# Kernel tuning notes

Measured on AMD Instinct MI355X. Metric: run time of the kernel, lower is better.

Reference implementation:

```python
import jax, jax.numpy as jnp
import numpy as np

HEADS = 16
HIDDEN = 1024
HEAD_DIM = HIDDEN // HEADS


def setup_inputs() -> dict:
    key = jax.random.key(0)
    ks = jax.random.split(key, 12)
    B, S, H = 2, 2048, HIDDEN
    scale = 1.0 / np.sqrt(H)
    inp = {
        'q': jax.random.normal(ks[0], (B, S, H), jnp.float32),
        'k': jax.random.normal(ks[1], (B, S, H), jnp.float32),
        'v': jax.random.normal(ks[2], (B, S, H), jnp.float32),
        'mask': jnp.ones((B, S), jnp.int32),
        'Wq': jax.random.normal(ks[3], (H, H), jnp.float32) * scale,
        'bq': jnp.zeros((H,), jnp.float32),
        'Wk': jax.random.normal(ks[4], (H, H), jnp.float32) * scale,
        'bk': jnp.zeros((H,), jnp.float32),
        'Wv': jax.random.normal(ks[5], (H, H), jnp.float32) * scale,
        'bv': jnp.zeros((H,), jnp.float32),
        'Wo': jax.random.normal(ks[6], (H, H), jnp.float32) * scale,
        'bo': jnp.zeros((H,), jnp.float32),
    }
    return inp


def reference(q, k, v, mask, Wq, bq, Wk, bk, Wv, bv, Wo, bo):
    B, S, H = q.shape
    hd = HEAD_DIM
    # projections (torch Linear: x @ W.T + b) -> [B, heads, S, hd]
    qh = (q @ Wq.T + bq).reshape(B, S, HEADS, hd).transpose(0, 2, 1, 3)
    kh = (k @ Wk.T + bk).reshape(B, S, HEADS, hd).transpose(0, 2, 1, 3)
    vh = (v @ Wv.T + bv).reshape(B, S, HEADS, hd).transpose(0, 2, 1, 3)
    # full score matrix [B, heads, Sq, Sk]
    scores = jnp.einsum('bhqd,bhkd->bhqk', qh, kh) / np.sqrt(hd)
    # mask [B, Sq] -> [B, 1, Sq, 1], masks entire query rows where mask==0
    m = mask[:, None, :, None]
    scores = jnp.where(m == 0, jnp.float32(-1e9), scores)
    attn = jax.nn.softmax(scores, axis=-1)
    # dropout omitted (eval mode / deterministic)
    y = jnp.einsum('bhqk,bhkd->bhqd', attn, vh)
    y = y.transpose(0, 2, 1, 3).reshape(B, S, H)
    return y @ Wo.T + bo
```

## Files before the change

### kernel.cpp

```cpp
#include <hip/hip_runtime.h>
#include <hip/hip_bf16.h>
#include <cstdint>

#define EL 1048576ull

typedef __bf16 bf16_t;
typedef bf16_t bf16x8 __attribute__((ext_vector_type(8)));
typedef float  f32x4  __attribute__((ext_vector_type(4)));
typedef unsigned int u32x2 __attribute__((ext_vector_type(2)));
typedef unsigned int u32x4 __attribute__((ext_vector_type(4)));

__device__ __forceinline__ unsigned short f2bf(float f) {
  unsigned int u = __builtin_bit_cast(unsigned int, f);
  u += 0x7FFFu + ((u >> 16) & 1u);
  return (unsigned short)(u >> 16);
}

__device__ __forceinline__ unsigned int cvtpk(float lo, float hi2) {
  unsigned int r;
  asm("v_cvt_pk_bf16_f32 %0, %1, %2" : "=v"(r) : "v"(lo), "v"(hi2));
  return r;
}

__device__ __forceinline__ float fexp2(float x) {
#if __has_builtin(__builtin_amdgcn_exp2f)
  return __builtin_amdgcn_exp2f(x);
#else
  return exp2f(x);
#endif
}

typedef __attribute__((address_space(1))) void as1_void;
typedef __attribute__((address_space(3))) void as3_void;
__device__ __forceinline__ void load_lds16(const void* g, void* l) {
  __builtin_amdgcn_global_load_lds((as1_void*)g, (as3_void*)l, 16, 0, 0);
}

__device__ __forceinline__ bf16x8 repack_af(const f32x4 s0v, const f32x4 s1v) {
  unsigned int c00 = cvtpk(s0v[0], s0v[1]);
  unsigned int c01 = cvtpk(s0v[2], s0v[3]);
  unsigned int c10 = cvtpk(s1v[0], s1v[1]);
  unsigned int c11 = cvtpk(s1v[2], s1v[3]);
  asm("v_permlane32_swap_b32 %0, %1" : "+v"(c00), "+v"(c10));
  asm("v_permlane16_swap_b32 %0, %1" : "+v"(c00), "+v"(c10));
  asm("v_permlane32_swap_b32 %0, %1" : "+v"(c01), "+v"(c11));
  asm("v_permlane16_swap_b32 %0, %1" : "+v"(c01), "+v"(c11));
  u32x4 wd; wd[0] = c00; wd[1] = c01; wd[2] = c10; wd[3] = c11;
  return __builtin_bit_cast(bf16x8, wd);
}

__global__ __launch_bounds__(256) void convert_all(
    const float* __restrict__ q, const float* __restrict__ k, const float* __restrict__ v,
    const float* __restrict__ wq, const float* __restrict__ wk,
    const float* __restrict__ wv, const float* __restrict__ wo,
    unsigned short* __restrict__ ws)
{
  const size_t total_v4 = 4 * EL;
  for (size_t v4 = (size_t)blockIdx.x * blockDim.x + threadIdx.x; v4 < total_v4;
       v4 += (size_t)gridDim.x * blockDim.x) {
    size_t e = v4 * 4;
    unsigned seg = (unsigned)(e >> 20);
    const float* s; size_t base;
    if      (seg < 4)   { s = q;  base = 0; }
    else if (seg < 8)   { s = k;  base = 4*EL; }
    else if (seg < 12)  { s = v;  base = 8*EL; }
    else if (seg == 12) { s = wq; base = 12*EL; }
    else if (seg == 13) { s = wk; base = 13*EL; }
    else if (seg == 14) { s = wv; base = 14*EL; }
    else                { s = wo; base = 15*EL; }
    const float4 f = *(const float4*)(s + (e - base));
    ushort4 o;
    o.x = f2bf(f.x); o.y = f2bf(f.y); o.z = f2bf(f.z); o.w = f2bf(f.w);
    *(ushort4*)(ws + e) = o;
  }
}

template <int BM, int BN, int WM, int WN>
__device__ __forceinline__ void gemm_bt_main(
    const unsigned short* __restrict__ A,
    const unsigned short* __restrict__ B,
    f32x4 (&acc)[BM / WM / 16][BN / WN / 16],
    const int tm, const int tn)
{
  constexpr int K = 1024, BK = 64;
  constexpr int AM = BM / WM / 16, AN = BN / WN / 16;
  __shared__ __align__(16) unsigned short sA[BM * BK];
  __shared__ __align__(16) unsigned short sB[BN * BK];
  const int tid  = threadIdx.x;
  const int wave = tid >> 6, lane = tid & 63;
  const int wm = wave / WN, wn = wave % WN;
  const int l16 = lane & 15, hi = lane >> 4, swz = l16 & 7;

  for (int k0 = 0; k0 < K; k0 += BK) {
    __syncthreads();
#pragma unroll
    for (int i = 0; i < BM * 8 / 256; i++) {
      int p = i * 256 + tid;
      int row = p >> 3, c = p & 7;
      load_lds16(A + (size_t)(tm + row) * K + k0 + ((c ^ (row & 7)) * 8),
                 &sA[(i * 256 + wave * 64) * 8]);
    }
#pragma unroll
    for (int i = 0; i < BN * 8 / 256; i++) {
      int p = i * 256 + tid;
      int row = p >> 3, c = p & 7;
      load_lds16(B + (size_t)(tn + row) * K + k0 + ((c ^ (row & 7)) * 8),
                 &sB[(i * 256 + wave * 64) * 8]);
    }
    __syncthreads();

#pragma unroll
    for (int kk = 0; kk < 2; kk++) {
      bf16x8 af[AM], bfr[AN];
#pragma unroll
      for (int i = 0; i < AM; i++) {
        int row = wm * (BM / WM) + i * 16 + l16;
        af[i] = *(const bf16x8*)&sA[row * BK + (((kk * 4 + hi) ^ swz) * 8)];
      }
#pragma unroll
      for (int j = 0; j < AN; j++) {
        int row = wn * (BN / WN) + j * 16 + l16;
        bfr[j] = *(const bf16x8*)&sB[row * BK + (((kk * 4 + hi) ^ swz) * 8)];
      }
#pragma unroll
      for (int i = 0; i < AM; i++)
#pragma unroll
        for (int j = 0; j < AN; j++)
          acc[i][j] = __builtin_amdgcn_mfma_f32_16x16x32_bf16(af[i], bfr[j], acc[i][j], 0, 0, 0);
    }
  }
}

__global__ __launch_bounds__(256, 3) void qkv_gemm(
    const unsigned short* qb, const unsigned short* kb, const unsigned short* vb,
    const unsigned short* wqb, const unsigned short* wkb, const unsigned short* wvb,
    const float* bq, const float* bk, const float* bv,
    unsigned short* Qp, unsigned short* Kp, unsigned short* Vt)
{
  const unsigned short* A; const unsigned short* B; const float* bias;
  if (blockIdx.z == 0)      { A = qb; B = wqb; bias = bq; }
  else if (blockIdx.z == 1) { A = kb; B = wkb; bias = bk; }
  else                      { A = vb; B = wvb; bias = bv; }

  const int xd = blockIdx.x, yd = blockIdx.y;
  const int mt = xd + 8 * (yd & 3);
  const int nt = yd >> 2;
  const int tm = mt * 128, tn = nt * 128;

  f32x4 acc[4][4] = {};
  gemm_bt_main<128, 128, 2, 2>(A, B, acc, tm, tn);

  const int tid = threadIdx.x, wave = tid >> 6, lane = tid & 63;
  const int wm = wave >> 1, wn = wave & 1;
  const int l16 = lane & 15, hi = lane >> 4;

  if (blockIdx.z < 2) {
    unsigned short* C = (blockIdx.z == 0) ? Qp : Kp;
    const float scale = (blockIdx.z == 0) ? 0.18033688011112042f : 1.0f;
#pragma unroll
    for (int i = 0; i < 4; i++) {
      int row0 = tm + wm * 64 + i * 16 + hi * 4;
#pragma unroll
      for (int j = 0; j < 4; j++) {
        int col = tn + wn * 64 + j * 16 + l16;
        float bv2 = bias[col];
#pragma unroll
        for (int r = 0; r < 4; r++)
          C[(size_t)(row0 + r) * 1024 + col] = f2bf((acc[i][j][r] + bv2) * scale);
      }
    }
  } else {
#pragma unroll
    for (int i = 0; i < 4; i++) {
      int row0 = tm + wm * 64 + i * 16 + hi * 4;
      int bb = row0 >> 11, s = row0 & 2047;
#pragma unroll
      for (int j = 0; j < 4; j++) {
        int col = tn + wn * 64 + j * 16 + l16;
        int hh = col >> 6, d = col & 63;
        float bv2 = bias[col];
        u32x2 w;
        w[0] = cvtpk(acc[i][j][0] + bv2, acc[i][j][1] + bv2);
        w[1] = cvtpk(acc[i][j][2] + bv2, acc[i][j][3] + bv2);
        *(u32x2*)&Vt[((size_t)(bb * 16 + hh) * 64 + d) * 2048 + s] = w;
      }
    }
  }
}

__global__ __launch_bounds__(256, 2) void out_gemm(
    const unsigned short* Yb, const unsigned short* wob, const float* bo, float* out)
{
  const int xd = blockIdx.x, yd = blockIdx.y;
  const int mt = (xd & 7) + 8 * (yd & 3);
  const int nt = (xd >> 3) + 2 * (yd >> 2);
  const int tm = mt * 128, tn = nt * 64;

  f32x4 acc[2][4] = {};
  gemm_bt_main<128, 64, 4, 1>(Yb, wob, acc, tm, tn);

  const int tid = threadIdx.x, wave = tid >> 6, lane = tid & 63;
  const int l16 = lane & 15, hi = lane >> 4;
#pragma unroll
  for (int i = 0; i < 2; i++) {
    int row0 = tm + wave * 32 + i * 16 + hi * 4;
#pragma unroll
    for (int j = 0; j < 4; j++) {
      int col = tn + j * 16 + l16;
      float bv2 = bo[col];
#pragma unroll
      for (int r = 0; r < 4; r++)
        out[(size_t)(row0 + r) * 1024 + col] = acc[i][j][r] + bv2;
    }
  }
}

__global__ __launch_bounds__(256, 2) void attn_kernel(
    const unsigned short* __restrict__ Qp, const unsigned short* __restrict__ Kp,
    const unsigned short* __restrict__ Vt, const int* __restrict__ mask,
    unsigned short* __restrict__ Yb)
{
  constexpr int S = 2048, H = 1024;
  __shared__ __align__(16) unsigned short sK[2][128 * 64];
  __shared__ __align__(16) unsigned short sV[2][64 * 128];

  const int tid = threadIdx.x, wave = tid >> 6, lane = tid & 63;
  const int l16 = lane & 15, hi = lane >> 4, swz = l16 & 7;
  const int xd = blockIdx.x, hd = blockIdx.y;
  const int h  = (xd & 7) + 8 * (hd & 1);
  const int qt = ((xd >> 3) + 2 * (hd >> 1)) * 128;
  const int b = blockIdx.z, bh = b * 16 + h;
  const unsigned short* Qb = Qp + (size_t)b * S * H + (size_t)h * 64;
  const unsigned short* Kb = Kp + (size_t)b * S * H + (size_t)h * 64;
  const unsigned short* Vb = Vt + (size_t)bh * 64 * 2048;

  const int kinv0 = l16 * 64 + ((hi ^ swz) * 8);
  const int kinv1 = l16 * 64 + (((4 + hi) ^ swz) * 8);
  const int vinv0 = l16 * 128 + ((hi ^ swz) * 8);
  const int vinv1 = l16 * 128 + (((4 + hi) ^ swz) * 8);

#pragma unroll
  for (int i = 0; i < 4; i++) {
    int p = i * 256 + tid, row = p >> 3, c = p & 7;
    load_lds16(Qb + (size_t)(qt + row) * H + ((c ^ (row & 7)) * 8),
               &sK[1][(i * 256 + wave * 64) * 8]);
  }
  const unsigned short* pK[4]; const unsigned short* pV[4];
#pragma unroll
  for (int j = 0; j < 4; j++) {
    int g = j * 256 + tid;
    int row = g >> 3, c = g & 7;
    pK[j] = Kb + (size_t)row * H + ((c ^ (row & 7)) * 8);
    int d = g >> 4, kvc = g & 15;
    int sg = ((kvc ^ d) & 7) | (kvc & 8);
    pV[j] = Vb + (size_t)d * 2048 + sg * 8;
  }
#pragma unroll
  for (int j = 0; j < 4; j++)
    load_lds16(pK[j], &sK[0][(j * 256 + wave * 64) * 8]);
#pragma unroll
  for (int j = 0; j < 4; j++)
    load_lds16(pV[j], &sV[0][(j * 256 + wave * 64) * 8]);
#pragma unroll
  for (int j = 0; j < 4; j++) { pK[j] += 128 * H; pV[j] += 128; }

  asm volatile("s_waitcnt vmcnt(8)" ::: "memory");
  __builtin_amdgcn_sched_barrier(0);
  __builtin_amdgcn_s_barrier();

  bf16x8 qf[2][2];
#pragma unroll
  for (int m = 0; m < 2; m++) {
    const int row = wave * 32 + m * 16 + l16;
    const int qm = mask[(size_t)b * S + qt + row];
#pragma unroll
    for (int ks = 0; ks < 2; ks++) {
      bf16x8 v = *(const bf16x8*)&sK[1][row * 64 + (((ks * 4 + hi) ^ swz) * 8)];
      u32x4 u = __builtin_bit_cast(u32x4, v);
#pragma unroll
      for (int c = 0; c < 4; c++) u[c] = qm ? u[c] : 0u;
      qf[m][ks] = __builtin_bit_cast(bf16x8, u);
    }
  }
  asm volatile("s_waitcnt lgkmcnt(0)" ::: "memory");
  __builtin_amdgcn_sched_barrier(0);
  __builtin_amdgcn_s_barrier();

  float lsum[2] = {0.f, 0.f};
  f32x4 oacc[2][4] = {};

  for (int t = 0; t < 16; t++) {
    const int cur = t & 1;
    if (t < 15) {
      unsigned short* nK = sK[cur ^ 1];
      unsigned short* nV = sV[cur ^ 1];
#pragma unroll
      for (int j = 0; j < 4; j++)
        load_lds16(pK[j], &nK[(j * 256 + wave * 64) * 8]);
#pragma unroll
      for (int j = 0; j < 4; j++)
        load_lds16(pV[j], &nV[(j * 256 + wave * 64) * 8]);
#pragma unroll
      for (int j = 0; j < 4; j++) { pK[j] += 128 * H; pV[j] += 128; }
      asm volatile("s_waitcnt vmcnt(8)" ::: "memory");
    } else {
      asm volatile("s_waitcnt vmcnt(0)" ::: "memory");
    }
    __builtin_amdgcn_sched_barrier(0);
    __builtin_amdgcn_s_barrier();

    const unsigned short* kb = sK[cur];
    const unsigned short* vb = sV[cur];

#pragma unroll
    for (int hf = 0; hf < 2; hf++) {
      f32x4 sf[2][4];
      __builtin_amdgcn_s_setprio(1);
#pragma unroll
      for (int jj = 0; jj < 4; jj++) {
        const int ro = (hf * 4 + jj) * 1024;
        bf16x8 kf0 = *(const bf16x8*)&kb[ro + kinv0];
        bf16x8 kf1 = *(const bf16x8*)&kb[ro + kinv1];
#pragma unroll
        for (int m = 0; m < 2; m++) {
          f32x4 acc = {-16.0f, -16.0f, -16.0f, -16.0f};
          acc = __builtin_amdgcn_mfma_f32_16x16x32_bf16(kf0, qf[m][0], acc, 0, 0, 0);
          acc = __builtin_amdgcn_mfma_f32_16x16x32_bf16(kf1, qf[m][1], acc, 0, 0, 0);
          sf[m][jj] = acc;
        }
      }
      __builtin_amdgcn_s_setprio(0);

#pragma unroll
      for (int m = 0; m < 2; m++) {
#pragma unroll
        for (int jj = 0; jj < 4; jj++)
#pragma unroll
          for (int r = 0; r < 4; r++)
            sf[m][jj][r] = fexp2(sf[m][jj][r]);
        f32x4 c4 = (sf[m][0] + sf[m][1]) + (sf[m][2] + sf[m][3]);
        lsum[m] += (c4[0] + c4[1]) + (c4[2] + c4[3]);
      }

#pragma unroll
      for (int w2 = 0; w2 < 2; w2++) {
        bf16x8 af0 = repack_af(sf[0][2 * w2], sf[0][2 * w2 + 1]);
        bf16x8 af1 = repack_af(sf[1][2 * w2], sf[1][2 * w2 + 1]);
        const int gw = hf * 2 + w2;
        const int vo = ((gw & 2) ? 64 : 0) + ((gw & 1) ? vinv1 : vinv0);
        __builtin_amdgcn_s_setprio(1);
#pragma unroll
        for (int n = 0; n < 4; n++) {
          bf16x8 vf = *(const bf16x8*)&vb[n * 2048 + vo];
          oacc[0][n] = __builtin_amdgcn_mfma_f32_16x16x32_bf16(af0, vf, oacc[0][n], 0, 0, 0);
          oacc[1][n] = __builtin_amdgcn_mfma_f32_16x16x32_bf16(af1, vf, oacc[1][n], 0, 0, 0);
        }
        __builtin_amdgcn_s_setprio(0);
      }
    }
    __builtin_amdgcn_sched_barrier(0);
    __builtin_amdgcn_s_barrier();
  }

#pragma unroll
  for (int m = 0; m < 2; m++) {
    lsum[m] += __shfl_xor(lsum[m], 16);
    lsum[m] += __shfl_xor(lsum[m], 32);
  }
#pragma unroll
  for (int m = 0; m < 2; m++) {
    float lr[4];
#pragma unroll
    for (int r = 0; r < 4; r++) lr[r] = 1.0f / __shfl(lsum[m], hi * 4 + r);
#pragma unroll
    for (int n = 0; n < 4; n++)
#pragma unroll
      for (int r = 0; r < 4; r++) {
        int row = qt + wave * 32 + m * 16 + hi * 4 + r;
        int col = n * 16 + l16;
        Yb[((size_t)b * S + row) * H + h * 64 + col] = f2bf(oacc[m][n][r] * lr[r]);
      }
  }
}

extern "C" void kernel_launch(void* const* d_in, const int* in_sizes, int n_in,
                              void* d_out, int out_size, void* d_ws, size_t ws_size,
                              hipStream_t stream)
{
  const float* q  = (const float*)d_in[0];
  const float* k  = (const float*)d_in[1];
  const float* v  = (const float*)d_in[2];
  const int*  mask = (const int*)d_in[3];
  const float* Wq = (const float*)d_in[4];
  const float* bq = (const float*)d_in[5];
  const float* Wk = (const float*)d_in[6];
  const float* bk = (const float*)d_in[7];
  const float* Wv = (const float*)d_in[8];
  const float* bv = (const float*)d_in[9];
  const float* Wo = (const float*)d_in[10];
  const float* bo = (const float*)d_in[11];

  unsigned short* ws  = (unsigned short*)d_ws;
  unsigned short* qb  = ws;
  unsigned short* kb  = ws + 4 * EL;
  unsigned short* vb  = ws + 8 * EL;
  unsigned short* wqb = ws + 12 * EL;
  unsigned short* wkb = ws + 13 * EL;
  unsigned short* wvb = ws + 14 * EL;
  unsigned short* wob = ws + 15 * EL;
  unsigned short* Qp  = ws + 16 * EL;
  unsigned short* Kp  = ws + 20 * EL;
  unsigned short* Vt  = ws + 24 * EL;
  unsigned short* Yb  = ws + 28 * EL;

  convert_all<<<2048, 256, 0, stream>>>(q, k, v, Wq, Wk, Wv, Wo, ws);
  qkv_gemm<<<dim3(8, 32, 3), 256, 0, stream>>>(qb, kb, vb, wqb, wkb, wvb,
                                               bq, bk, bv, Qp, Kp, Vt);
  attn_kernel<<<dim3(16, 16, 2), 256, 0, stream>>>(Qp, Kp, Vt, mask, Yb);
  out_gemm<<<dim3(16, 32), 256, 0, stream>>>(Yb, wob, bo, (float*)d_out);
}
```

Measured before the change: 108.3 us.

## Split attention KV sequence across two wave groups with LDS reduction

Doubles the attention block to 512 threads: two groups of four waves each process half of the key/value sequence for the same 128-query tile, using per-half 64-row double-buffered K/V tiles in LDS. At the end, the second half writes its partial output and row sums to shared memory and the first half combines them before normalising and writing bf16 output. This aims to raise per-CU wave parallelism and latency hiding for the attention loop, at the cost of an extra LDS reduction, a block-wide sync and higher register/LDS pressure per block, which may limit occupancy.

```diff
diff --git a/kernel.cpp b/kernel.cpp
--- a/kernel.cpp
+++ b/kernel.cpp
@@ -215,17 +215,18 @@
   }
 }
 
-__global__ __launch_bounds__(256, 2) void attn_kernel(
+__global__ __launch_bounds__(512, 2) void attn_kernel(
     const unsigned short* __restrict__ Qp, const unsigned short* __restrict__ Kp,
     const unsigned short* __restrict__ Vt, const int* __restrict__ mask,
     unsigned short* __restrict__ Yb)
 {
   constexpr int S = 2048, H = 1024;
-  __shared__ __align__(16) unsigned short sK[2][128 * 64];
-  __shared__ __align__(16) unsigned short sV[2][64 * 128];
+  __shared__ __align__(16) unsigned short smem[32768];
 
   const int tid = threadIdx.x, wave = tid >> 6, lane = tid & 63;
   const int l16 = lane & 15, hi = lane >> 4, swz = l16 & 7;
+  const int half = wave >> 2, w4 = wave & 3;
+  const int kvoff = half * 1024;
   const int xd = blockIdx.x, hd = blockIdx.y;
   const int h  = (xd & 7) + 8 * (hd & 1);
   const int qt = ((xd >> 3) + 2 * (hd >> 1)) * 128;
@@ -234,48 +235,59 @@
   const unsigned short* Kb = Kp + (size_t)b * S * H + (size_t)h * 64;
   const unsigned short* Vb = Vt + (size_t)bh * 64 * 2048;
 
+  unsigned short* sK0 = smem + (half * 2) * 4096;
+  unsigned short* sK1 = smem + (half * 2 + 1) * 4096;
+  unsigned short* sV0 = smem + 16384 + (half * 2) * 4096;
+  unsigned short* sV1 = smem + 16384 + (half * 2 + 1) * 4096;
+
   const int kinv0 = l16 * 64 + ((hi ^ swz) * 8);
   const int kinv1 = l16 * 64 + (((4 + hi) ^ swz) * 8);
-  const int vinv0 = l16 * 128 + ((hi ^ swz) * 8);
-  const int vinv1 = l16 * 128 + (((4 + hi) ^ swz) * 8);
-
-#pragma unroll
-  for (int i = 0; i < 4; i++) {
-    int p = i * 256 + tid, row = p >> 3, c = p & 7;
-    load_lds16(Qb + (size_t)(qt + row) * H + ((c ^ (row & 7)) * 8),
-               &sK[1][(i * 256 + wave * 64) * 8]);
-  }
-  const unsigned short* pK[4]; const unsigned short* pV[4];
-#pragma unroll
-  for (int j = 0; j < 4; j++) {
-    int g = j * 256 + tid;
+  const int vinv0 = kinv0, vinv1 = kinv1;
+
+  {
+    unsigned short* qdst0 = smem + 4096;
+    unsigned short* qdst1 = smem + 12288;
+#pragma unroll
+    for (int i = 0; i < 2; i++) {
+      int p = i * 512 + tid, row = p >> 3, c = p & 7;
+      load_lds16(Qb + (size_t)(qt + row) * H + ((c ^ (row & 7)) * 8),
+                 &(i ? qdst1 : qdst0)[(wave * 64) * 8]);
+    }
+  }
+  const int htid = tid & 255;
+  const unsigned short* pK[2]; const unsigned short* pV[2];
+#pragma unroll
+  for (int j = 0; j < 2; j++) {
+    int g = j * 256 + htid;
     int row = g >> 3, c = g & 7;
-    pK[j] = Kb + (size_t)row * H + ((c ^ (row & 7)) * 8);
-    int d = g >> 4, kvc = g & 15;
-    int sg = ((kvc ^ d) & 7) | (kvc & 8);
-    pV[j] = Vb + (size_t)d * 2048 + sg * 8;
-  }
-#pragma unroll
-  for (int j = 0; j < 4; j++)
-    load_lds16(pK[j], &sK[0][(j * 256 + wave * 64) * 8]);
-#pragma unroll
-  for (int j = 0; j < 4; j++)
-    load_lds16(pV[j], &sV[0][(j * 256 + wave * 64) * 8]);
-#pragma unroll
-  for (int j = 0; j < 4; j++) { pK[j] += 128 * H; pV[j] += 128; }
-
-  asm volatile("s_waitcnt vmcnt(8)" ::: "memory");
+    pK[j] = Kb + (size_t)(kvoff + row) * H + ((c ^ (row & 7)) * 8);
+    int d = g >> 3, kvc = g & 7;
+    int sg = kvc ^ (d & 7);
+    pV[j] = Vb + (size_t)d * 2048 + kvoff + sg * 8;
+  }
+#pragma unroll
+  for (int j = 0; j < 2; j++)
+    load_lds16(pK[j], &sK0[(j * 256 + w4 * 64) * 8]);
+#pragma unroll
+  for (int j = 0; j < 2; j++)
+    load_lds16(pV[j], &sV0[(j * 256 + w4 * 64) * 8]);
+#pragma unroll
+  for (int j = 0; j < 2; j++) { pK[j] += 64 * H; pV[j] += 64; }
+
+  asm volatile("s_waitcnt vmcnt(4)" ::: "memory");
   __builtin_amdgcn_sched_barrier(0);
   __builtin_amdgcn_s_barrier();
 
   bf16x8 qf[2][2];
 #pragma unroll
   for (int m = 0; m < 2; m++) {
-    const int row = wave * 32 + m * 16 + l16;
+    const int row = w4 * 32 + m * 16 + l16;
     const int qm = mask[(size_t)b * S + qt + row];
+    const unsigned short* qsrc = (row < 64) ? (smem + 4096 + row * 64)
+                                            : (smem + 12288 + (row - 64) * 64);
 #pragma unroll
     for (int ks = 0; ks < 2; ks++) {
-      bf16x8 v = *(const bf16x8*)&sK[1][row * 64 + (((ks * 4 + hi) ^ swz) * 8)];
+      bf16x8 v = *(const bf16x8*)&qsrc[((ks * 4 + hi) ^ swz) * 8];
       u32x4 u = __builtin_bit_cast(u32x4, v);
 #pragma unroll
       for (int c = 0; c < 4; c++) u[c] = qm ? u[c] : 0u;
@@ -292,71 +304,67 @@
   for (int t = 0; t < 16; t++) {
     const int cur = t & 1;
     if (t < 15) {
-      unsigned short* nK = sK[cur ^ 1];
-      unsigned short* nV = sV[cur ^ 1];
-#pragma unroll
-      for (int j = 0; j < 4; j++)
-        load_lds16(pK[j], &nK[(j * 256 + wave * 64) * 8]);
-#pragma unroll
-      for (int j = 0; j < 4; j++)
-        load_lds16(pV[j], &nV[(j * 256 + wave * 64) * 8]);
-#pragma unroll
-      for (int j = 0; j < 4; j++) { pK[j] += 128 * H; pV[j] += 128; }
-      asm volatile("s_waitcnt vmcnt(8)" ::: "memory");
+      unsigned short* nK = cur ? sK0 : sK1;
+      unsigned short* nV = cur ? sV0 : sV1;
+#pragma unroll
+      for (int j = 0; j < 2; j++)
+        load_lds16(pK[j], &nK[(j * 256 + w4 * 64) * 8]);
+#pragma unroll
+      for (int j = 0; j < 2; j++)
+        load_lds16(pV[j], &nV[(j * 256 + w4 * 64) * 8]);
+#pragma unroll
+      for (int j = 0; j < 2; j++) { pK[j] += 64 * H; pV[j] += 64; }
+      asm volatile("s_waitcnt vmcnt(4)" ::: "memory");
     } else {
       asm volatile("s_waitcnt vmcnt(0)" ::: "memory");
     }
     __builtin_amdgcn_sched_barrier(0);
     __builtin_amdgcn_s_barrier();
 
-    const unsigned short* kb = sK[cur];
-    const unsigned short* vb = sV[cur];
-
-#pragma unroll
-    for (int hf = 0; hf < 2; hf++) {
-      f32x4 sf[2][4];
+    const unsigned short* kb = cur ? sK1 : sK0;
+    const unsigned short* vb = cur ? sV1 : sV0;
+
+    f32x4 sf[2][4];
+    __builtin_amdgcn_s_setprio(1);
+#pragma unroll
+    for (int jj = 0; jj < 4; jj++) {
+      const int ro = jj * 1024;
+      bf16x8 kf0 = *(const bf16x8*)&kb[ro + kinv0];
+      bf16x8 kf1 = *(const bf16x8*)&kb[ro + kinv1];
+#pragma unroll
+      for (int m = 0; m < 2; m++) {
+        f32x4 acc = {-16.0f, -16.0f, -16.0f, -16.0f};
+        acc = __builtin_amdgcn_mfma_f32_16x16x32_bf16(kf0, qf[m][0], acc, 0, 0, 0);
+        acc = __builtin_amdgcn_mfma_f32_16x16x32_bf16(kf1, qf[m][1], acc, 0, 0, 0);
+        sf[m][jj] = acc;
+      }
+    }
+    __builtin_amdgcn_s_setprio(0);
+
+#pragma unroll
+    for (int m = 0; m < 2; m++) {
+#pragma unroll
+      for (int jj = 0; jj < 4; jj++)
+#pragma unroll
+        for (int r = 0; r < 4; r++)
+          sf[m][jj][r] = fexp2(sf[m][jj][r]);
+      f32x4 c4 = (sf[m][0] + sf[m][1]) + (sf[m][2] + sf[m][3]);
+      lsum[m] += (c4[0] + c4[1]) + (c4[2] + c4[3]);
+    }
+
+#pragma unroll
+    for (int w2 = 0; w2 < 2; w2++) {
+      bf16x8 af0 = repack_af(sf[0][2 * w2], sf[0][2 * w2 + 1]);
+      bf16x8 af1 = repack_af(sf[1][2 * w2], sf[1][2 * w2 + 1]);
+      const int vo = w2 ? vinv1 : vinv0;
       __builtin_amdgcn_s_setprio(1);
 #pragma unroll
-      for (int jj = 0; jj < 4; jj++) {
-        const int ro = (hf * 4 + jj) * 1024;
-        bf16x8 kf0 = *(const bf16x8*)&kb[ro + kinv0];
-        bf16x8 kf1 = *(const bf16x8*)&kb[ro + kinv1];
-#pragma unroll
-        for (int m = 0; m < 2; m++) {
-          f32x4 acc = {-16.0f, -16.0f, -16.0f, -16.0f};
-          acc = __builtin_amdgcn_mfma_f32_16x16x32_bf16(kf0, qf[m][0], acc, 0, 0, 0);
-          acc = __builtin_amdgcn_mfma_f32_16x16x32_bf16(kf1, qf[m][1], acc, 0, 0, 0);
-          sf[m][jj] = acc;
-        }
+      for (int n = 0; n < 4; n++) {
+        bf16x8 vf = *(const bf16x8*)&vb[n * 1024 + vo];
+        oacc[0][n] = __builtin_amdgcn_mfma_f32_16x16x32_bf16(af0, vf, oacc[0][n], 0, 0, 0);
+        oacc[1][n] = __builtin_amdgcn_mfma_f32_16x16x32_bf16(af1, vf, oacc[1][n], 0, 0, 0);
       }
       __builtin_amdgcn_s_setprio(0);
-
-#pragma unroll
-      for (int m = 0; m < 2; m++) {
-#pragma unroll
-        for (int jj = 0; jj < 4; jj++)
-#pragma unroll
-          for (int r = 0; r < 4; r++)
-            sf[m][jj][r] = fexp2(sf[m][jj][r]);
-        f32x4 c4 = (sf[m][0] + sf[m][1]) + (sf[m][2] + sf[m][3]);
-        lsum[m] += (c4[0] + c4[1]) + (c4[2] + c4[3]);
-      }
-
-#pragma unroll
-      for (int w2 = 0; w2 < 2; w2++) {
-        bf16x8 af0 = repack_af(sf[0][2 * w2], sf[0][2 * w2 + 1]);
-        bf16x8 af1 = repack_af(sf[1][2 * w2], sf[1][2 * w2 + 1]);
-        const int gw = hf * 2 + w2;
-        const int vo = ((gw & 2) ? 64 : 0) + ((gw & 1) ? vinv1 : vinv0);
-        __builtin_amdgcn_s_setprio(1);
-#pragma unroll
-        for (int n = 0; n < 4; n++) {
-          bf16x8 vf = *(const bf16x8*)&vb[n * 2048 + vo];
-          oacc[0][n] = __builtin_amdgcn_mfma_f32_16x16x32_bf16(af0, vf, oacc[0][n], 0, 0, 0);
-          oacc[1][n] = __builtin_amdgcn_mfma_f32_16x16x32_bf16(af1, vf, oacc[1][n], 0, 0, 0);
-        }
-        __builtin_amdgcn_s_setprio(0);
-      }
     }
     __builtin_amdgcn_sched_barrier(0);
     __builtin_amdgcn_s_barrier();
@@ -367,19 +375,41 @@
     lsum[m] += __shfl_xor(lsum[m], 16);
     lsum[m] += __shfl_xor(lsum[m], 32);
   }
-#pragma unroll
-  for (int m = 0; m < 2; m++) {
-    float lr[4];
-#pragma unroll
-    for (int r = 0; r < 4; r++) lr[r] = 1.0f / __shfl(lsum[m], hi * 4 + r);
-#pragma unroll
-    for (int n = 0; n < 4; n++)
-#pragma unroll
-      for (int r = 0; r < 4; r++) {
-        int row = qt + wave * 32 + m * 16 + hi * 4 + r;
-        int col = n * 16 + l16;
-        Yb[((size_t)b * S + row) * H + h * 64 + col] = f2bf(oacc[m][n][r] * lr[r]);
-      }
+
+  float* sO = (float*)smem;
+  float* sL = (float*)(smem + 16896);
+
+  if (half == 1) {
+#pragma unroll
+    for (int m = 0; m < 2; m++) {
+      if (hi == 0) sL[w4 * 32 + m * 16 + l16] = lsum[m];
+#pragma unroll
+      for (int n = 0; n < 4; n++)
+#pragma unroll
+        for (int r = 0; r < 4; r++) {
+          int qq = w4 * 32 + m * 16 + hi * 4 + r;
+          sO[qq * 66 + n * 16 + l16] = oacc[m][n][r];
+        }
+    }
+  }
+  __syncthreads();
+  if (half == 0) {
+#pragma unroll
+    for (int m = 0; m < 2; m++) {
+      float lt = lsum[m] + sL[w4 * 32 + m * 16 + l16];
+      float lr[4];
+#pragma unroll
+      for (int r = 0; r < 4; r++) lr[r] = 1.0f / __shfl(lt, hi * 4 + r);
+#pragma unroll
+      for (int n = 0; n < 4; n++)
+#pragma unroll
+        for (int r = 0; r < 4; r++) {
+          int qq = w4 * 32 + m * 16 + hi * 4 + r;
+          int col = n * 16 + l16;
+          float val = (oacc[m][n][r] + sO[qq * 66 + col]) * lr[r];
+          Yb[((size_t)b * S + qt + qq) * H + h * 64 + col] = f2bf(val);
+        }
+    }
   }
 }
 
@@ -416,6 +446,6 @@
   convert_all<<<2048, 256, 0, stream>>>(q, k, v, Wq, Wk, Wv, Wo, ws);
   qkv_gemm<<<dim3(8, 32, 3), 256, 0, stream>>>(qb, kb, vb, wqb, wkb, wvb,
                                                bq, bk, bv, Qp, Kp, Vt);
-  attn_kernel<<<dim3(16, 16, 2), 256, 0, stream>>>(Qp, Kp, Vt, mask, Yb);
+  attn_kernel<<<dim3(16, 16, 2), 512, 0, stream>>>(Qp, Kp, Vt, mask, Yb);
   out_gemm<<<dim3(16, 32), 256, 0, stream>>>(Yb, wob, bo, (float*)d_out);
 }
```

New measurement: 104.8 us. -3.2%, faster.
